# Kernel optimization log

Measured on AMD Instinct MI355X. Metric: run time of the kernel, lower is better.

Reference implementation:

```python
import jax, jax.numpy as jnp
import numpy as np

B, C, N, K = 2, 64, 8192, 16


def conv1d(x, W, b):  # x [B,Cin,N], W [Cout,Cin]
    return jnp.einsum('oc,bcn->bon', W, x) + b[None, :, None]


def conv2d(x, W, b):  # x [B,Cin,N,K], W [Cout,Cin]
    return jnp.einsum('oc,bcnk->bonk', W, x) + b[None, :, None, None]


def bn1(x, s, t):  # eval-mode BN folded to affine, [B,C,N]
    return x * s[None, :, None] + t[None, :, None]


def bn2(x, s, t):  # [B,C,N,K]
    return x * s[None, :, None, None] + t[None, :, None, None]


def knn_idx(p, k):  # p [B,N,3] -> [B,N,k] nearest (incl. self)
    sq = jnp.sum(p * p, axis=-1)
    d = sq[:, :, None] + sq[:, None, :] - 2.0 * jnp.einsum('bnd,bmd->bnm', p, p)
    _, idx = jax.lax.top_k(-d, k)
    return idx


def group(f, idx):  # f [B,C,N], idx [B,N,K] -> [B,C,N,K]
    return jax.vmap(lambda fb, ib: fb[:, ib])(f, idx)


def setup_inputs() -> dict:
    key = jax.random.key(0)
    ks = jax.random.split(key, 16)
    s = 0.05
    inp = {
        'input_p': jax.random.normal(ks[0], (B, 3, N), jnp.float32),
        'input_x': jax.random.normal(ks[1], (B, C, N), jnp.float32),
        'W_top': jax.random.normal(ks[2], (C, C), jnp.float32) * s,
        'b_top': jnp.zeros((C,), jnp.float32),
        's_top': jnp.ones((C,), jnp.float32),
        't_top': jnp.zeros((C,), jnp.float32),
        'W_phi': jax.random.normal(ks[3], (C, C), jnp.float32) * s,
        'b_phi': jnp.zeros((C,), jnp.float32),
        'W_psi': jax.random.normal(ks[4], (C, C), jnp.float32) * s,
        'b_psi': jnp.zeros((C,), jnp.float32),
        'W_alpha': jax.random.normal(ks[5], (C, C), jnp.float32) * s,
        'b_alpha': jnp.zeros((C,), jnp.float32),
        'W_g1': jax.random.normal(ks[6], (C, C), jnp.float32) * s,
        'b_g1': jnp.zeros((C,), jnp.float32),
        's_g1': jnp.ones((C,), jnp.float32),
        't_g1': jnp.zeros((C,), jnp.float32),
        'W_g2': jax.random.normal(ks[7], (C, C), jnp.float32) * s,
        'b_g2': jnp.zeros((C,), jnp.float32),
        's_g2': jnp.ones((C,), jnp.float32),
        't_g2': jnp.zeros((C,), jnp.float32),
        'W_d1': jax.random.normal(ks[8], (C, 3), jnp.float32) * s,
        'b_d1': jnp.zeros((C,), jnp.float32),
        's_d1': jnp.ones((C,), jnp.float32),
        't_d1': jnp.zeros((C,), jnp.float32),
        'W_d2': jax.random.normal(ks[9], (C, C), jnp.float32) * s,
        'b_d2': jnp.zeros((C,), jnp.float32),
        's_d2': jnp.ones((C,), jnp.float32),
        't_d2': jnp.zeros((C,), jnp.float32),
        'W_down': jax.random.normal(ks[10], (C, C), jnp.float32) * s,
        'b_down': jnp.zeros((C,), jnp.float32),
        's_down': jnp.ones((C,), jnp.float32),
        't_down': jnp.zeros((C,), jnp.float32),
    }
    return inp


def reference(input_p, input_x, W_top, b_top, s_top, t_top, W_phi, b_phi,
              W_psi, b_psi, W_alpha, b_alpha, W_g1, b_g1, s_g1, t_g1,
              W_g2, b_g2, s_g2, t_g2, W_d1, b_d1, s_d1, t_d1,
              W_d2, b_d2, s_d2, t_d2, W_down, b_down, s_down, t_down):
    p = jnp.transpose(input_p, (0, 2, 1))            # [B,N,3]
    idx = knn_idx(p, K)                              # [B,N,K]
    grouped_p = group(input_p, idx)                  # [B,3,N,K]

    x = bn1(conv1d(input_x, W_top, b_top), s_top, t_top)
    phi = conv1d(x, W_phi, b_phi)                    # [B,C,N]
    psi_g = group(conv1d(x, W_psi, b_psi), idx)      # [B,C,N,K]
    alpha_g = group(conv1d(x, W_alpha, b_alpha), idx)

    rel = input_p[:, :, :, None] - grouped_p         # [B,3,N,K]
    pos = bn2(conv2d(jax.nn.relu(bn2(conv2d(rel, W_d1, b_d1), s_d1, t_d1)),
                     W_d2, b_d2), s_d2, t_d2)        # [B,C,N,K]

    pre = phi[:, :, :, None] - psi_g + pos
    g = bn2(conv2d(jax.nn.relu(bn2(conv2d(pre, W_g1, b_g1), s_g1, t_g1)),
                   W_g2, b_g2), s_g2, t_g2)
    attn = jax.nn.softmax(g, axis=-1)                # softmax over neighbors

    y = jnp.sum(attn * (alpha_g + pos), axis=-1)     # [B,C,N]
    out = bn1(conv1d(y, W_down, b_down), s_down, t_down) + input_x
    return out, attn
```

## Files before the change

kernel.cpp:

```cpp
#include <hip/hip_runtime.h>
#include <cfloat>

#define BN 16384

#define WOFF_WT    0
#define WOFF_P1M   4096
#define WOFF_G1M   8192
#define WOFF_MMT   12288
#define WOFF_WD2T  16384
#define WOFF_G2T   20480
#define WOFF_WDN   24576
#define WOFF_WAL   28672
#define WOFF_WD1   32768
#define WOFF_BT    33024
#define WOFF_BAL   33088
#define WOFF_VC    33152
#define WOFF_UD1   33216
#define WOFF_UD2   33280
#define WOFF_UDN   33344
#define WOFF_WMB   33792
#define WOFF_WD2B  35840
#define WOFF_G2B   37888
#define WB         39936

static constexpr size_t OFF_P1   = WB;
static constexpr size_t OFF_G1   = OFF_P1 + (size_t)BN*64;
static constexpr size_t OFF_AL   = OFF_G1 + (size_t)BN*64;
static constexpr size_t OFF_R1   = OFF_AL + (size_t)BN*64;
static constexpr size_t OFF_P4   = OFF_R1 + (size_t)BN*64;
static constexpr size_t OFF_IDX  = OFF_P4 + (size_t)BN*4;
static constexpr size_t OFF_Y    = OFF_IDX + (size_t)BN*16;

struct P32 { const float* a[32]; };

#define WSWZ(i,o) ((o) ^ (((i)&7)<<2))

typedef __attribute__((ext_vector_type(8))) short bf16x8;
typedef __attribute__((ext_vector_type(4))) float f32x4;

__device__ __forceinline__ unsigned bf2(float lo, float hi) {
  unsigned a = __float_as_uint(lo); a = (a + 0x7fffu + ((a>>16)&1u)) >> 16;
  unsigned b = __float_as_uint(hi); b = (b + 0x7fffu + ((b>>16)&1u)) & 0xffff0000u;
  return a | b;
}

__global__ __launch_bounds__(256) void k0_fold(P32 P, float* __restrict__ ws)
{
  const int bid = blockIdx.x, tid = threadIdx.x;
  const float* Wtop = P.a[2];  const float* btop = P.a[3];
  const float* stop = P.a[4];  const float* ttop = P.a[5];
  const float* Wphi = P.a[6];  const float* bphi = P.a[7];
  const float* Wpsi = P.a[8];  const float* bpsi = P.a[9];
  const float* Wal  = P.a[10]; const float* bal  = P.a[11];
  const float* Wg1  = P.a[12]; const float* bg1  = P.a[13];
  const float* sg1  = P.a[14]; const float* tg1  = P.a[15];
  const float* Wg2  = P.a[16];
  const float* sg2  = P.a[18];
  const float* Wd1  = P.a[20]; const float* bd1  = P.a[21];
  const float* sd1  = P.a[22]; const float* td1  = P.a[23];
  const float* Wd2  = P.a[24]; const float* bd2  = P.a[25];
  const float* sd2  = P.a[26]; const float* td2  = P.a[27];
  const float* Wdn  = P.a[28]; const float* bdn  = P.a[29];
  const float* sdn  = P.a[30]; const float* tdn  = P.a[31];

  if (bid == 0) {
    for (int e = tid; e < 4096; e += 256) { int o = e >> 6; ws[WOFF_WT + e] = stop[o]*Wtop[e]; }
    if (tid < 64) {
      ws[WOFF_BT  + tid] = stop[tid]*btop[tid] + ttop[tid];
      ws[WOFF_BAL + tid] = bal[tid];
      ws[WOFF_UD1 + tid] = sd1[tid]*bd1[tid] + td1[tid];
      ws[WOFF_UD2 + tid] = sd2[tid]*bd2[tid] + td2[tid];
      ws[WOFF_UDN + tid] = sdn[tid]*bdn[tid] + tdn[tid];
      float acc = 0.f;
      for (int c = 0; c < 64; ++c)
        acc += Wg1[tid*64+c] * (bphi[c] - bpsi[c] + sd2[c]*bd2[c] + td2[c]);
      ws[WOFF_VC + tid] = sg1[tid]*(acc + bg1[tid]) + tg1[tid];
    }
  } else if (bid == 1) {
    for (int e = tid; e < 4096; e += 256) {
      int o = e >> 6, i = e & 63; float a = 0.f;
      for (int c = 0; c < 64; ++c) a += Wg1[o*64+c]*Wphi[c*64+i];
      ws[WOFF_P1M + e] = sg1[o]*a;
    }
  } else if (bid == 2) {
    for (int e = tid; e < 4096; e += 256) {
      int o = e >> 6, i = e & 63; float a = 0.f;
      for (int c = 0; c < 64; ++c) a += Wg1[o*64+c]*Wpsi[c*64+i];
      ws[WOFF_G1M + e] = sg1[o]*a;
    }
  } else if (bid == 3) {
    for (int e = tid; e < 4096; e += 256) {
      int cp = e >> 6, c = e & 63; float a = 0.f;
      for (int u = 0; u < 64; ++u) a += Wg1[c*64+u]*sd2[u]*Wd2[u*64+cp];
      ws[WOFF_MMT + e] = sg1[c]*a;
    }
  } else if (bid == 4) {
    for (int e = tid; e < 4096; e += 256) {
      int cp = e >> 6, c = e & 63;
      ws[WOFF_WD2T + e] = sd2[c]*Wd2[c*64+cp];
    }
    if (tid < 192) ws[WOFF_WD1 + tid] = sd1[tid/3]*Wd1[tid];
  } else if (bid == 5) {
    for (int e = tid; e < 4096; e += 256) {
      int cp = e >> 6, c = e & 63;
      ws[WOFF_G2T + e] = sg2[c]*Wg2[c*64+cp];
    }
  } else if (bid == 6) {
    for (int e = tid; e < 4096; e += 256) { int o = e >> 6; ws[WOFF_WDN + e] = sdn[o]*Wdn[e]; }
  } else {
    for (int e = tid; e < 4096; e += 256) ws[WOFF_WAL + e] = Wal[e];
  }
}

__global__ __launch_bounds__(256) void k0b_pack(float* __restrict__ ws)
{
  const int m = blockIdx.x;
  const int srcO = (m==0) ? WOFF_MMT : (m==1) ? WOFF_WD2T : WOFF_G2T;
  const int dstO = (m==0) ? WOFF_WMB : (m==1) ? WOFF_WD2B : WOFF_G2B;
  unsigned* dst = (unsigned*)&ws[dstO];
  for (int w = threadIdx.x; w < 2048; w += 256) {
    int c = w >> 5, pair = w & 31;
    float v0 = ws[srcO + (pair*2  )*64 + c];
    float v1 = ws[srcO + (pair*2+1)*64 + c];
    dst[w] = bf2(v0, v1);
  }
}

__global__ __launch_bounds__(256) void k1_feat(const float* __restrict__ inp,
                                               const float* __restrict__ inx,
                                               float* __restrict__ ws)
{
  __shared__ float tX[64][16];
  __shared__ float wT[64][64];
  const int tid = threadIdx.x;
  const int pt = tid & 15, q = tid >> 4;
  const int gid0 = blockIdx.x * 16;
  const int b = gid0 >> 13, n0 = gid0 & 8191;
  const size_t gq = (size_t)gid0 + pt;

  for (int r = tid; r < 1024; r += 256) {
    int c = r >> 4, col = r & 15;
    tX[c][col] = inx[((size_t)(b*64 + c) << 13) + n0 + col];
  }
  for (int r = tid; r < 4096; r += 256) {
    int o = r >> 6, i = r & 63;
    wT[i][WSWZ(i,o)] = ws[WOFF_WT + r];
  }
  __syncthreads();

  float acc[4];
  #pragma unroll
  for (int i = 0; i < 4; ++i) acc[i] = ws[WOFF_BT + q*4 + i];
  for (int ci = 0; ci < 64; ++ci) {
    float xv = tX[ci][pt];
    const float4 w4 = *(const float4*)&wT[ci][WSWZ(ci, q*4)];
    acc[0] = fmaf(w4.x, xv, acc[0]);
    acc[1] = fmaf(w4.y, xv, acc[1]);
    acc[2] = fmaf(w4.z, xv, acc[2]);
    acc[3] = fmaf(w4.w, xv, acc[3]);
  }
  __syncthreads();
  #pragma unroll
  for (int i = 0; i < 4; ++i) tX[q*4 + i][pt] = acc[i];

  {
    size_t pb = (size_t)b*3*8192 + n0 + pt;
    float px = inp[pb], py = inp[pb + 8192], pz = inp[pb + 16384];
    float sq = __fadd_rn(__fadd_rn(__fmul_rn(px,px), __fmul_rn(py,py)), __fmul_rn(pz,pz));
    if (q == 0) *(float4*)&ws[OFF_P4 + gq*4] = make_float4(px,py,pz,sq);
    float r1v[4];
    #pragma unroll
    for (int i = 0; i < 4; ++i) {
      int c = q*4 + i;
      float a = ws[WOFF_WD1 + c*3+0]*px;
      a = fmaf(ws[WOFF_WD1 + c*3+1], py, a);
      a = fmaf(ws[WOFF_WD1 + c*3+2], pz, a);
      r1v[i] = a;
    }
    *(float4*)&ws[OFF_R1 + gq*64 + q*4] = make_float4(r1v[0], r1v[1], r1v[2], r1v[3]);
  }
  __syncthreads();

  #pragma unroll
  for (int m = 0; m < 3; ++m) {
    const int    mof = (m==0) ? WOFF_P1M : (m==1) ? WOFF_G1M : WOFF_WAL;
    const size_t oof = (m==0) ? OFF_P1   : (m==1) ? OFF_G1   : OFF_AL;
    __syncthreads();
    for (int r = tid; r < 4096; r += 256) {
      int o = r >> 6, i = r & 63;
      wT[i][WSWZ(i,o)] = ws[mof + r];
    }
    __syncthreads();
    #pragma unroll
    for (int i = 0; i < 4; ++i) acc[i] = (m == 2) ? ws[WOFF_BAL + q*4 + i] : 0.f;
    for (int ci = 0; ci < 64; ++ci) {
      float xv = tX[ci][pt];
      const float4 w4 = *(const float4*)&wT[ci][WSWZ(ci, q*4)];
      acc[0] = fmaf(w4.x, xv, acc[0]);
      acc[1] = fmaf(w4.y, xv, acc[1]);
      acc[2] = fmaf(w4.z, xv, acc[2]);
      acc[3] = fmaf(w4.w, xv, acc[3]);
    }
    *(float4*)&ws[oof + gq*64 + q*4] = make_float4(acc[0], acc[1], acc[2], acc[3]);
  }
}

__device__ __forceinline__ float pdist(const float4 q4, const float4 c4) {
  float m = __fadd_rn(__fadd_rn(__fmul_rn(q4.x,c4.x), __fmul_rn(q4.y,c4.y)), __fmul_rn(q4.z,c4.z));
  return __fsub_rn(__fadd_rn(q4.w, c4.w), __fmul_rn(2.f, m));
}

__global__ __launch_bounds__(256) void k2_topk(float* __restrict__ ws)
{
  __shared__ float4 tile[1024];
  const int tid = threadIdx.x;
  const int lane = tid & 63, w = tid >> 6;
  const int gid = blockIdx.x*4 + w;
  const int b = gid >> 13;
  const float4 q4 = *(const float4*)&ws[OFF_P4 + (size_t)gid*4];
  const float4* cp4 = (const float4*)&ws[OFF_P4 + (size_t)b*8192*4];

  unsigned long long heap  = ~0ull;
  unsigned long long worst = ~0ull;

  #pragma unroll 1
  for (int c0 = 0; c0 < 8192; c0 += 1024) {
    __syncthreads();
    #pragma unroll
    for (int t = 0; t < 4; ++t) tile[tid + t*256] = cp4[c0 + tid + t*256];
    __syncthreads();
    #pragma unroll 1
    for (int r = 0; r < 16; ++r) {
      const int ci = r*64 + lane;
      float d = pdist(q4, tile[ci]);
      unsigned db = __float_as_uint(d);
      db ^= ((int)db < 0) ? 0xffffffffu : 0x80000000u;
      unsigned long long key = ((unsigned long long)db << 32) | (unsigned)(c0 + ci);
      unsigned long long mask = __ballot(key < worst);
      while (mask) {
        const int src = __ffsll((long long)mask) - 1;
        mask &= mask - 1ull;
        const unsigned long long k = __shfl(key, src);
        if (k < worst) {
          unsigned long long prev = __shfl_up(heap, 1);
          heap = (heap <= k) ? heap : ((lane == 0 || prev <= k) ? k : prev);
          worst = __shfl(heap, 15);
        }
      }
    }
  }
  if (lane < 16)
    ((int*)&ws[OFF_IDX])[(size_t)gid*16 + lane] = (int)(unsigned)(heap & 0xffffffffu);
}

__global__ __launch_bounds__(256) void k3_mfma(float* __restrict__ ws, float* __restrict__ out)
{
  __shared__ __align__(16) unsigned char wL[24576];
  __shared__ __align__(16) unsigned char hL[32768];
  const int tid = threadIdx.x;
  const int lane = tid & 63, wid = tid >> 6;
  const int l15 = lane & 15, hi = lane >> 4;
  const int gid0 = blockIdx.x * 16;
  const int b = gid0 >> 13;
  const int n0 = gid0 & 8191;

  {
    const uint4* wsrc = (const uint4*)&ws[WOFF_WMB];
    for (int t = tid; t < 1536; t += 256) {
      int m = t >> 9, r = t & 511;
      int c = r >> 3, q = r & 7;
      uint4 v = wsrc[t];
      *(uint4*)(wL + m*8192 + ((c*128 + q*16) ^ ((c&7)<<4))) = v;
    }
  }
  {
    const int pt = tid >> 4, kq = tid & 15;
    const size_t gq = (size_t)gid0 + pt;
    const int jh = ((const int*)&ws[OFF_IDX])[gq*16 + kq];
    const size_t gjh = (size_t)b*8192 + jh;
    const float4* Ar = (const float4*)&ws[OFF_R1 + gq*64];
    const float4* Br = (const float4*)&ws[OFF_R1 + gjh*64];
    const float4* Ur = (const float4*)&ws[WOFF_UD1];
    const int swzh = (tid & 7) << 4;
    #pragma unroll
    for (int t = 0; t < 16; ++t) {
      float4 a = Ar[t], bb = Br[t], u = Ur[t];
      float v0 = fmaxf(a.x - bb.x + u.x, 0.f);
      float v1 = fmaxf(a.y - bb.y + u.y, 0.f);
      float v2 = fmaxf(a.z - bb.z + u.z, 0.f);
      float v3 = fmaxf(a.w - bb.w + u.w, 0.f);
      *(uint2*)(hL + ((tid*128 + t*8) ^ swzh)) = make_uint2(bf2(v0,v1), bf2(v2,v3));
    }
  }
  __syncthreads();

  float* attnp = out + (size_t)2*64*8192;
  const f32x4 zf = {0.f, 0.f, 0.f, 0.f};

  for (int i = 0; i < 4; ++i) {
    const int ct = (wid << 2) + i;
    const int n = n0 + ct;
    const size_t gqc = (size_t)gid0 + ct;
    const int mycol = (ct << 4) + l15;
    const int swz = (mycol & 7) << 4;
    const int hbase = mycol*128 + hi*16;
    bf16x8 hb0 = *(const bf16x8*)(hL + ((hbase     ) ^ swz));
    bf16x8 hb1 = *(const bf16x8*)(hL + ((hbase + 64) ^ swz));
    const int jj = ((const int*)&ws[OFF_IDX])[gqc*16 + l15];
    const size_t gjc = (size_t)b*8192 + jj;

    f32x4 accD[4], accM[4];
    #pragma unroll
    for (int rt = 0; rt < 4; ++rt) { accD[rt] = zf; accM[rt] = zf; }
    #pragma unroll
    for (int rt = 0; rt < 4; ++rt) {
      const int c = (rt << 4) + l15;
      const int ws2 = (c & 7) << 4;
      const int wb = c*128 + hi*16;
      bf16x8 m0 = *(const bf16x8*)(wL + (((wb     ) ^ ws2)));
      bf16x8 m1 = *(const bf16x8*)(wL + (((wb + 64) ^ ws2)));
      bf16x8 d0 = *(const bf16x8*)(wL + (8192 + ((wb     ) ^ ws2)));
      bf16x8 d1 = *(const bf16x8*)(wL + (8192 + ((wb + 64) ^ ws2)));
      accM[rt] = __builtin_amdgcn_mfma_f32_16x16x32_bf16(m0, hb0, accM[rt], 0, 0, 0);
      accM[rt] = __builtin_amdgcn_mfma_f32_16x16x32_bf16(m1, hb1, accM[rt], 0, 0, 0);
      accD[rt] = __builtin_amdgcn_mfma_f32_16x16x32_bf16(d0, hb0, accD[rt], 0, 0, 0);
      accD[rt] = __builtin_amdgcn_mfma_f32_16x16x32_bf16(d1, hb1, accD[rt], 0, 0, 0);
    }

    #pragma unroll
    for (int rt = 0; rt < 4; ++rt) {
      const int c0 = (rt << 4) + (hi << 2);
      const float4 p1 = *(const float4*)&ws[OFF_P1 + gqc*64 + c0];
      const float4 g1 = *(const float4*)&ws[OFF_G1 + gjc*64 + c0];
      const float4 vc = *(const float4*)&ws[WOFF_VC + c0];
      float h0 = fmaxf(accM[rt][0] + p1.x - g1.x + vc.x, 0.f);
      float h1 = fmaxf(accM[rt][1] + p1.y - g1.y + vc.y, 0.f);
      float h2 = fmaxf(accM[rt][2] + p1.z - g1.z + vc.z, 0.f);
      float h3 = fmaxf(accM[rt][3] + p1.w - g1.w + vc.w, 0.f);
      *(uint2*)(hL + ((mycol*128 + (c0 << 1)) ^ swz)) = make_uint2(bf2(h0,h1), bf2(h2,h3));
    }

    bf16x8 gb0 = *(const bf16x8*)(hL + ((hbase     ) ^ swz));
    bf16x8 gb1 = *(const bf16x8*)(hL + ((hbase + 64) ^ swz));
    f32x4 accG[4];
    #pragma unroll
    for (int rt = 0; rt < 4; ++rt) accG[rt] = zf;
    #pragma unroll
    for (int rt = 0; rt < 4; ++rt) {
      const int c = (rt << 4) + l15;
      const int ws2 = (c & 7) << 4;
      const int wb = c*128 + hi*16;
      bf16x8 g0 = *(const bf16x8*)(wL + (16384 + ((wb     ) ^ ws2)));
      bf16x8 g1f = *(const bf16x8*)(wL + (16384 + ((wb + 64) ^ ws2)));
      accG[rt] = __builtin_amdgcn_mfma_f32_16x16x32_bf16(g0,  gb0, accG[rt], 0, 0, 0);
      accG[rt] = __builtin_amdgcn_mfma_f32_16x16x32_bf16(g1f, gb1, accG[rt], 0, 0, 0);
    }

    #pragma unroll
    for (int rt = 0; rt < 4; ++rt) {
      const int c0 = (rt << 4) + (hi << 2);
      const float4 al = *(const float4*)&ws[OFF_AL + gjc*64 + c0];
      const float4 u2 = *(const float4*)&ws[WOFF_UD2 + c0];
      float y4[4];
      #pragma unroll
      for (int r = 0; r < 4; ++r) {
        float g = accG[rt][r];
        float mx = g;
        mx = fmaxf(mx, __shfl_xor(mx, 1));
        mx = fmaxf(mx, __shfl_xor(mx, 2));
        mx = fmaxf(mx, __shfl_xor(mx, 4));
        mx = fmaxf(mx, __shfl_xor(mx, 8));
        float e = __expf(g - mx);
        float sm = e;
        sm += __shfl_xor(sm, 1);
        sm += __shfl_xor(sm, 2);
        sm += __shfl_xor(sm, 4);
        sm += __shfl_xor(sm, 8);
        float rs;
        asm("v_rcp_f32 %0, %1" : "=v"(rs) : "v"(sm));
        float a = e * rs;
        attnp[(((size_t)(b*64 + c0 + r) << 13) + n)*16 + l15] = a;
        float pv = ((const float*)&al)[r] + accD[rt][r] + ((const float*)&u2)[r];
        float yv = a * pv;
        yv += __shfl_xor(yv, 1);
        yv += __shfl_xor(yv, 2);
        yv += __shfl_xor(yv, 4);
        yv += __shfl_xor(yv, 8);
        y4[r] = yv;
      }
      if (l15 == 0)
        *(float4*)&ws[OFF_Y + gqc*64 + c0] = make_float4(y4[0], y4[1], y4[2], y4[3]);
    }
  }
}

__global__ __launch_bounds__(256) void k4_out(const float* __restrict__ inx,
                                              float* __restrict__ ws,
                                              float* __restrict__ out)
{
  __shared__ float yS[16][64];
  __shared__ float wT[64][64];
  const int tid = threadIdx.x;
  const int pt = tid & 15, q = tid >> 4;
  const int gid0 = blockIdx.x*16;
  const int b = gid0 >> 13, n0 = gid0 & 8191;
  for (int r = tid; r < 1024; r += 256) {
    int p2 = r >> 6, c = r & 63;
    yS[p2][c ^ p2] = ws[OFF_Y + (size_t)(gid0 + p2)*64 + c];
  }
  for (int r = tid; r < 4096; r += 256) {
    int o = r >> 6, i = r & 63;
    wT[i][WSWZ(i,o)] = ws[WOFF_WDN + r];
  }
  __syncthreads();
  float acc[4];
  #pragma unroll
  for (int i = 0; i < 4; ++i) acc[i] = ws[WOFF_UDN + q*4 + i];
  for (int ci = 0; ci < 64; ++ci) {
    float yv = yS[pt][ci ^ pt];
    const float4 w4 = *(const float4*)&wT[ci][WSWZ(ci, q*4)];
    acc[0] = fmaf(w4.x, yv, acc[0]);
    acc[1] = fmaf(w4.y, yv, acc[1]);
    acc[2] = fmaf(w4.z, yv, acc[2]);
    acc[3] = fmaf(w4.w, yv, acc[3]);
  }
  #pragma unroll
  for (int i = 0; i < 4; ++i) {
    const int c = q*4 + i;
    size_t o = ((size_t)(b*64 + c) << 13) + n0 + pt;
    out[o] = acc[i] + inx[o];
  }
}

extern "C" void kernel_launch(void* const* d_in, const int* in_sizes, int n_in,
                              void* d_out, int out_size, void* d_ws, size_t ws_size,
                              hipStream_t stream)
{
  (void)in_sizes; (void)n_in; (void)out_size; (void)ws_size;
  float* ws = (float*)d_ws;
  const float* inp = (const float*)d_in[0];
  const float* inx = (const float*)d_in[1];
  float* out = (float*)d_out;
  P32 P;
  for (int i = 0; i < 32; ++i) P.a[i] = (const float*)d_in[i];

  k0_fold   <<<8,      256, 0, stream>>>(P, ws);
  k0b_pack  <<<3,      256, 0, stream>>>(ws);
  k1_feat   <<<BN/16,  256, 0, stream>>>(inp, inx, ws);
  k2_topk   <<<BN/4,   256, 0, stream>>>(ws);
  k3_mfma   <<<BN/16,  256, 0, stream>>>(ws, out);
  k4_out    <<<BN/16,  256, 0, stream>>>(inx, ws, out);
}
```

Baseline: 315.2 us.

## Replace warp-serial top-k heap with histogram threshold filter and candidate select

The kNN top-k kernel now builds a per-wave distance histogram over the first 1024 candidates and uses it to pick a threshold that at least 16 candidates fall under. It then compacts every candidate below that threshold into shared memory and extracts the 16 smallest with 16 wave-wide min reductions. This is meant to replace the ballot/shuffle heap insertion loop, which serialises across lanes. If more than 512 candidates pass the threshold, a slow single-lane full scan runs as a fallback. The histogram bins are tuned to the expected distance range, so other point distributions could hit that fallback often.

Result: slower. 1.090 ms (+245.7%).

```diff
diff --git a/kernel.cpp b/kernel.cpp
--- a/kernel.cpp
+++ b/kernel.cpp
@@ -210,47 +210,134 @@
   return __fsub_rn(__fadd_rn(q4.w, c4.w), __fmul_rn(2.f, m));
 }
 
+__device__ __forceinline__ unsigned dmono(float d) {
+  unsigned db = __float_as_uint(d);
+  return db ^ (((int)db < 0) ? 0xffffffffu : 0x80000000u);
+}
+
 __global__ __launch_bounds__(256) void k2_topk(float* __restrict__ ws)
 {
   __shared__ float4 tile[1024];
+  __shared__ unsigned long long buf[4][512];
+  __shared__ unsigned hist[4][64];
+  __shared__ unsigned cnt[4];
   const int tid = threadIdx.x;
   const int lane = tid & 63, w = tid >> 6;
   const int gid = blockIdx.x*4 + w;
   const int b = gid >> 13;
   const float4 q4 = *(const float4*)&ws[OFF_P4 + (size_t)gid*4];
   const float4* cp4 = (const float4*)&ws[OFF_P4 + (size_t)b*8192*4];
-
-  unsigned long long heap  = ~0ull;
-  unsigned long long worst = ~0ull;
+  int* ib = (int*)&ws[OFF_IDX];
+
+  hist[w][lane] = 0u;
+  if (tid < 4) cnt[tid] = 0u;
+  #pragma unroll
+  for (int t = 0; t < 4; ++t) tile[tid + t*256] = cp4[tid + t*256];
+  __syncthreads();
+
+  #pragma unroll 1
+  for (int r = 0; r < 16; ++r) {
+    float d = pdist(q4, tile[r*64 + lane]);
+    unsigned dbits = __float_as_uint(fmaxf(d, 0.f));
+    int bin = (int)(dbits >> 22) - 204;
+    bin = max(0, min(63, bin));
+    atomicAdd(&hist[w][bin], 1u);
+  }
+  unsigned ps = hist[w][lane];
+  #pragma unroll
+  for (int s = 1; s < 64; s <<= 1) {
+    unsigned o = __shfl_up(ps, s);
+    if (lane >= s) ps += o;
+  }
+  unsigned long long m16 = __ballot(ps >= 16u);
+  const int binT = (m16 == 0ull) ? 63 : (__ffsll((long long)m16) - 1);
+  const float T = (binT >= 63) ? FLT_MAX : __uint_as_float((unsigned)(binT + 205) << 22);
 
   #pragma unroll 1
   for (int c0 = 0; c0 < 8192; c0 += 1024) {
-    __syncthreads();
-    #pragma unroll
-    for (int t = 0; t < 4; ++t) tile[tid + t*256] = cp4[c0 + tid + t*256];
-    __syncthreads();
+    if (c0) {
+      __syncthreads();
+      #pragma unroll
+      for (int t = 0; t < 4; ++t) tile[tid + t*256] = cp4[c0 + tid + t*256];
+      __syncthreads();
+    }
+    #pragma unroll 1
+    for (int g = 0; g < 4; ++g) {
+      float dv[4];
+      unsigned sm = 0u;
+      #pragma unroll
+      for (int j = 0; j < 4; ++j) {
+        dv[j] = pdist(q4, tile[(g*4 + j)*64 + lane]);
+        if (dv[j] < T) sm |= (1u << j);
+      }
+      if (sm) {
+        unsigned pos = atomicAdd(&cnt[w], (unsigned)__popc(sm));
+        #pragma unroll
+        for (int j = 0; j < 4; ++j) if (sm & (1u << j)) {
+          unsigned p2 = pos + (unsigned)__popc(sm & ((1u << j) - 1u));
+          if (p2 < 512u)
+            buf[w][p2] = ((unsigned long long)dmono(dv[j]) << 32)
+                       | (unsigned)(c0 + (g*4 + j)*64 + lane);
+        }
+      }
+    }
+  }
+
+  const unsigned E = cnt[w];
+  if (E <= 512u) {
+    unsigned long long e0, e1, e2, e3, e4, e5, e6, e7;
+    e0 = (lane       < (int)E) ? buf[w][lane      ] : ~0ull;
+    e1 = (lane +  64 < (int)E) ? buf[w][lane +  64] : ~0ull;
+    e2 = (lane + 128 < (int)E) ? buf[w][lane + 128] : ~0ull;
+    e3 = (lane + 192 < (int)E) ? buf[w][lane + 192] : ~0ull;
+    e4 = (lane + 256 < (int)E) ? buf[w][lane + 256] : ~0ull;
+    e5 = (lane + 320 < (int)E) ? buf[w][lane + 320] : ~0ull;
+    e6 = (lane + 384 < (int)E) ? buf[w][lane + 384] : ~0ull;
+    e7 = (lane + 448 < (int)E) ? buf[w][lane + 448] : ~0ull;
+    unsigned myres = 0u;
     #pragma unroll 1
     for (int r = 0; r < 16; ++r) {
-      const int ci = r*64 + lane;
-      float d = pdist(q4, tile[ci]);
-      unsigned db = __float_as_uint(d);
-      db ^= ((int)db < 0) ? 0xffffffffu : 0x80000000u;
-      unsigned long long key = ((unsigned long long)db << 32) | (unsigned)(c0 + ci);
-      unsigned long long mask = __ballot(key < worst);
-      while (mask) {
-        const int src = __ffsll((long long)mask) - 1;
-        mask &= mask - 1ull;
-        const unsigned long long k = __shfl(key, src);
-        if (k < worst) {
-          unsigned long long prev = __shfl_up(heap, 1);
-          heap = (heap <= k) ? heap : ((lane == 0 || prev <= k) ? k : prev);
-          worst = __shfl(heap, 15);
+      unsigned long long a01 = (e0 < e1) ? e0 : e1;
+      unsigned long long a23 = (e2 < e3) ? e2 : e3;
+      unsigned long long a45 = (e4 < e5) ? e4 : e5;
+      unsigned long long a67 = (e6 < e7) ? e6 : e7;
+      unsigned long long a03 = (a01 < a23) ? a01 : a23;
+      unsigned long long a47 = (a45 < a67) ? a45 : a67;
+      unsigned long long m = (a03 < a47) ? a03 : a47;
+      #pragma unroll
+      for (int s = 1; s < 64; s <<= 1) {
+        unsigned long long o = __shfl_xor(m, s);
+        m = (o < m) ? o : m;
+      }
+      e0 = (e0 == m) ? ~0ull : e0;  e1 = (e1 == m) ? ~0ull : e1;
+      e2 = (e2 == m) ? ~0ull : e2;  e3 = (e3 == m) ? ~0ull : e3;
+      e4 = (e4 == m) ? ~0ull : e4;  e5 = (e5 == m) ? ~0ull : e5;
+      e6 = (e6 == m) ? ~0ull : e6;  e7 = (e7 == m) ? ~0ull : e7;
+      if (lane == r) myres = (unsigned)(m & 0xffffffffu);
+    }
+    if (lane < 16) ib[(size_t)gid*16 + lane] = (int)myres;
+  } else {
+    if (lane == 0) {
+      float ds[16]; int is[16];
+      #pragma unroll
+      for (int r = 0; r < 16; ++r) { ds[r] = FLT_MAX; is[r] = 0x7fffffff; }
+      for (int t = 0; t < 8192; ++t) {
+        float d = pdist(q4, cp4[t]);
+        if (d < ds[15]) {
+          #pragma unroll
+          for (int s = 15; s >= 0; --s) {
+            bool bs = d < ds[s];
+            bool bm = (s > 0) ? (d < ds[s-1]) : false;
+            float dn = bs ? (bm ? ds[s-1] : d) : ds[s];
+            int   jn = bs ? (bm ? is[s-1] : t) : is[s];
+            ds[s] = dn; is[s] = jn;
+          }
         }
       }
-    }
-  }
-  if (lane < 16)
-    ((int*)&ws[OFF_IDX])[(size_t)gid*16 + lane] = (int)(unsigned)(heap & 0xffffffffu);
+      #pragma unroll
+      for (int r = 0; r < 16; ++r) ib[(size_t)gid*16 + r] = is[r];
+    }
+  }
 }
 
 __global__ __launch_bounds__(256) void k3_mfma(float* __restrict__ ws, float* __restrict__ out)
```

## Replace wave-serial kNN heap insertion with per-lane top-5 lists and wave merge

Applied to the files above, without the earlier changes.

The old kNN kernel kept one 16-entry sorted list spread across the wave and inserted candidates one at a time through ballot and shuffle loops. Now each lane keeps its own sorted top-5 in registers, and the wave then merges these lists with 16 rounds of butterfly min-reductions. If any lane's fifth-best key could belong to the global top-16, a single-lane brute-force scan runs as an exact fallback. This removes the divergent serial insertion loop, at the cost of more register pressure and an occasional very slow fallback path.

Result: no change. 312.0 us (-1.0%).

```diff
diff --git a/kernel.cpp b/kernel.cpp
--- a/kernel.cpp
+++ b/kernel.cpp
@@ -210,6 +210,23 @@
   return __fsub_rn(__fadd_rn(q4.w, c4.w), __fmul_rn(2.f, m));
 }
 
+__device__ __forceinline__ unsigned dmono(float d) {
+  unsigned db = __float_as_uint(d);
+  return db ^ (((int)db < 0) ? 0xffffffffu : 0x80000000u);
+}
+
+__device__ __forceinline__ void ins5(unsigned long long& k0, unsigned long long& k1,
+                                     unsigned long long& k2, unsigned long long& k3,
+                                     unsigned long long& k4, unsigned long long x)
+{
+  unsigned long long t;
+  t = (k0 < x) ? k0 : x;  x = (k0 < x) ? x : k0;  k0 = t;
+  t = (k1 < x) ? k1 : x;  x = (k1 < x) ? x : k1;  k1 = t;
+  t = (k2 < x) ? k2 : x;  x = (k2 < x) ? x : k2;  k2 = t;
+  t = (k3 < x) ? k3 : x;  x = (k3 < x) ? x : k3;  k3 = t;
+  k4 = (k4 < x) ? k4 : x;
+}
+
 __global__ __launch_bounds__(256) void k2_topk(float* __restrict__ ws)
 {
   __shared__ float4 tile[1024];
@@ -219,9 +236,9 @@
   const int b = gid >> 13;
   const float4 q4 = *(const float4*)&ws[OFF_P4 + (size_t)gid*4];
   const float4* cp4 = (const float4*)&ws[OFF_P4 + (size_t)b*8192*4];
-
-  unsigned long long heap  = ~0ull;
-  unsigned long long worst = ~0ull;
+  int* ib = (int*)&ws[OFF_IDX];
+
+  unsigned long long k0=~0ull, k1=~0ull, k2=~0ull, k3=~0ull, k4=~0ull;
 
   #pragma unroll 1
   for (int c0 = 0; c0 < 8192; c0 += 1024) {
@@ -233,24 +250,57 @@
     for (int r = 0; r < 16; ++r) {
       const int ci = r*64 + lane;
       float d = pdist(q4, tile[ci]);
-      unsigned db = __float_as_uint(d);
-      db ^= ((int)db < 0) ? 0xffffffffu : 0x80000000u;
-      unsigned long long key = ((unsigned long long)db << 32) | (unsigned)(c0 + ci);
-      unsigned long long mask = __ballot(key < worst);
-      while (mask) {
-        const int src = __ffsll((long long)mask) - 1;
-        mask &= mask - 1ull;
-        const unsigned long long k = __shfl(key, src);
-        if (k < worst) {
-          unsigned long long prev = __shfl_up(heap, 1);
-          heap = (heap <= k) ? heap : ((lane == 0 || prev <= k) ? k : prev);
-          worst = __shfl(heap, 15);
+      unsigned long long x = ((unsigned long long)dmono(d) << 32) | (unsigned)(c0 + ci);
+      ins5(k0, k1, k2, k3, k4, x);
+    }
+  }
+
+  const unsigned long long savedk4 = k4;
+
+  unsigned myres = 0u;
+  unsigned long long m = 0ull;
+  #pragma unroll 1
+  for (int r = 0; r < 16; ++r) {
+    unsigned long long a01 = (k0 < k1) ? k0 : k1;
+    unsigned long long a23 = (k2 < k3) ? k2 : k3;
+    unsigned long long a03 = (a01 < a23) ? a01 : a23;
+    m = (a03 < k4) ? a03 : k4;
+    #pragma unroll
+    for (int s = 1; s < 64; s <<= 1) {
+      unsigned long long o = __shfl_xor(m, s);
+      m = (o < m) ? o : m;
+    }
+    k0 = (k0 == m) ? ~0ull : k0;  k1 = (k1 == m) ? ~0ull : k1;
+    k2 = (k2 == m) ? ~0ull : k2;  k3 = (k3 == m) ? ~0ull : k3;
+    k4 = (k4 == m) ? ~0ull : k4;
+    if (lane == r) myres = (unsigned)(m & 0xffffffffu);
+  }
+
+  const bool unsafe = __ballot(savedk4 < m) != 0ull;
+  if (!unsafe) {
+    if (lane < 16) ib[(size_t)gid*16 + lane] = (int)myres;
+  } else {
+    if (lane == 0) {
+      float ds[16]; int is[16];
+      #pragma unroll
+      for (int r = 0; r < 16; ++r) { ds[r] = FLT_MAX; is[r] = 0x7fffffff; }
+      for (int t = 0; t < 8192; ++t) {
+        float d = pdist(q4, cp4[t]);
+        if (d < ds[15]) {
+          #pragma unroll
+          for (int s = 15; s >= 0; --s) {
+            bool bs = d < ds[s];
+            bool bm = (s > 0) ? (d < ds[s-1]) : false;
+            float dn = bs ? (bm ? ds[s-1] : d) : ds[s];
+            int   jn = bs ? (bm ? is[s-1] : t) : is[s];
+            ds[s] = dn; is[s] = jn;
+          }
         }
       }
-    }
-  }
-  if (lane < 16)
-    ((int*)&ws[OFF_IDX])[(size_t)gid*16 + lane] = (int)(unsigned)(heap & 0xffffffffu);
+      #pragma unroll
+      for (int r = 0; r < 16; ++r) ib[(size_t)gid*16 + r] = is[r];
+    }
+  }
 }
 
 __global__ __launch_bounds__(256) void k3_mfma(float* __restrict__ ws, float* __restrict__ out)
```
